# Kernel optimization log

Hardware: AMD Instinct MI355X
Metric: run time of the kernel (lower is better)

Reference implementation:

```python
import jax, jax.numpy as jnp
import numpy as np

LAMBDA_DISCO = 1.0
THRESHOLD = 0.5
EPS = 1e-8
N = 8192


def setup_inputs() -> dict:
    key = jax.random.key(0)
    k1, k2, k3 = jax.random.split(key, 3)
    inputs = jax.random.normal(k1, (N, 1), dtype=jnp.float32)
    targets = jax.random.uniform(k2, (N, 1), dtype=jnp.float32)
    spectators = jax.random.uniform(k3, (N,), dtype=jnp.float32)
    return {"inputs": inputs, "targets": targets, "spectators": spectators}


def _masked_distance_correlation(x, y, m, c):
    """Distance correlation restricted to samples where mask m==1.

    Mathematically identical to filtering x[m], y[m] and running the dense
    dCor (cdist -> double-center -> mean of products), but with fixed shapes
    so it is jit-compatible. c = number of selected samples (>=1).
    """
    # 1-D pairwise L2 distances == |x_i - x_j|   [n, n]
    dx = jnp.abs(x[:, None] - x[None, :])
    dy = jnp.abs(y[:, None] - y[None, :])

    def double_center(D):
        row = (D @ m) / c          # masked row means  [n]
        col = (m @ D) / c          # masked col means  [n]
        tot = (m @ row) / c        # masked total mean (scalar)
        return D - row[:, None] - col[None, :] + tot

    cx = double_center(dx)
    cy = double_center(dy)
    M = m[:, None] * m[None, :]    # pairwise selection mask

    def masked_mean_prod(a, b):
        return jnp.sum(M * a * b) / (c * c)

    dcov_xy = jnp.sqrt(jnp.maximum(masked_mean_prod(cx, cy), EPS))
    dvar_x = jnp.sqrt(jnp.maximum(masked_mean_prod(cx, cx), EPS))
    dvar_y = jnp.sqrt(jnp.maximum(masked_mean_prod(cy, cy), EPS))
    return dcov_xy / (dvar_x * dvar_y)


def reference(inputs, targets, spectators):
    # BCEWithLogitsLoss (mean reduction), numerically stable form.
    x, t = inputs, targets
    bce = jnp.mean(jnp.maximum(x, 0.0) - x * t + jnp.log1p(jnp.exp(-jnp.abs(x))))

    probs = jax.nn.sigmoid(x).reshape(-1)                 # [n]
    m = (spectators >= THRESHOLD).astype(probs.dtype)     # [n] 0/1 mask
    count = jnp.sum(m)
    c_safe = jnp.maximum(count, 1.0)

    dcor = _masked_distance_correlation(probs, spectators, m, c_safe)
    # If no sample passes the condition, return plain BCE.
    return bce + LAMBDA_DISCO * jnp.where(count > 0, dcor, 0.0)
```

## Files before the change

kernel.cpp:

```cpp
#include <hip/hip_runtime.h>
#include <math.h>

#define NTOT 8192
#define THRESH 0.5f
#define EPS_F 1e-8f

#define NSEG 32
#define SEGSZ 256
#define NJG 8
#define SEG_PER_JG (NSEG / NJG)

#define OFF_CNT 0
#define OFF_BCEP 32
#define OFF_TXY 64
#define OFF_TXX 65
#define OFF_TYY 66
#define OFF_SUMS 67
#define OFF_DONE 72
#define OFF_PSS 128
#define OFF_RXP (OFF_PSS + 2 * NTOT)
#define OFF_RYP (OFF_RXP + NJG * NTOT)

__device__ inline float wave_reduce(float v) {
#pragma unroll
    for (int o = 32; o > 0; o >>= 1) v += __shfl_down(v, o, 64);
    return v;
}

__global__ void __launch_bounds__(256) k_stage1(const float* __restrict__ x,
                                                const float* __restrict__ t,
                                                const float* __restrict__ s,
                                                float* __restrict__ ws) {
    __shared__ unsigned wcnt[4];
    __shared__ float wbce[4];
    const int tid = threadIdx.x, b = blockIdx.x;
    const int lane = tid & 63, w = tid >> 6;
    if (b == 0 && tid < 16) ws[OFF_TXY + tid] = 0.f;

    const int i = b * SEGSZ + tid;
    float xi = x[i], ti = t[i], si = s[i];
    float bce = fmaxf(xi, 0.f) - xi * ti + log1pf(expf(-fabsf(xi)));
    bool sel = (si >= THRESH);
    unsigned long long ball = __ballot(sel);
    unsigned pre = __popcll(ball & ((1ull << lane) - 1ull));
    if (lane == 0) wcnt[w] = __popcll(ball);
    float bsum = wave_reduce(bce);
    if (lane == 0) wbce[w] = bsum;
    __syncthreads();
    unsigned off = 0;
#pragma unroll
    for (int k = 0; k < 4; ++k)
        if (k < w) off += wcnt[k];
    if (sel) {
        float p = 1.f / (1.f + expf(-xi));
        ((float2*)(ws + OFF_PSS))[b * SEGSZ + off + pre] = make_float2(p, si);
    }
    if (tid == 0) {
        ((unsigned*)(ws + OFF_CNT))[b] = wcnt[0] + wcnt[1] + wcnt[2] + wcnt[3];
        ws[OFF_BCEP + b] = wbce[0] + wbce[1] + wbce[2] + wbce[3];
    }
}

__global__ void __launch_bounds__(256) k_pairs(float* __restrict__ ws) {
    __shared__ float2 pjs[SEGSZ];
    __shared__ float accs[3];
    const int tid = threadIdx.x;
    const int ib = blockIdx.x & (NSEG - 1);
    const int jg = blockIdx.x >> 5;
    const unsigned* cnt = (const unsigned*)(ws + OFF_CNT);
    const float2* pss = (const float2*)(ws + OFF_PSS);
    const int ci = (int)cnt[ib];
    const bool valid = tid < ci;
    float2 me = valid ? pss[ib * SEGSZ + tid] : make_float2(0.f, 0.f);
    if (tid < 3) accs[tid] = 0.f;

    float rsx = 0.f, rsy = 0.f, t_xy = 0.f, t_xx = 0.f, t_yy = 0.f;
    for (int k = 0; k < SEG_PER_JG; ++k) {
        const int seg = jg * SEG_PER_JG + k;
        const int cj = (int)cnt[seg];
        __syncthreads();
        if (tid < cj) pjs[tid] = pss[seg * SEGSZ + tid];
        __syncthreads();
        if (valid) {
#pragma unroll 8
            for (int j = 0; j < cj; ++j) {
                float2 v = pjs[j];
                float d1 = me.x - v.x;
                float d2 = me.y - v.y;
                float a1 = fabsf(d1);
                float a2 = fabsf(d2);
                rsx += a1;
                rsy += a2;
                t_xy = fmaf(a1, a2, t_xy);
                t_xx = fmaf(d1, d1, t_xx);
                t_yy = fmaf(d2, d2, t_yy);
            }
        }
    }
    const int i = ib * SEGSZ + tid;
    ws[OFF_RXP + jg * NTOT + i] = rsx;
    ws[OFF_RYP + jg * NTOT + i] = rsy;

    t_xy = wave_reduce(t_xy);
    t_xx = wave_reduce(t_xx);
    t_yy = wave_reduce(t_yy);
    if ((tid & 63) == 0) {
        atomicAdd(&accs[0], t_xy);
        atomicAdd(&accs[1], t_xx);
        atomicAdd(&accs[2], t_yy);
    }
    __syncthreads();
    if (tid == 0) {
        atomicAdd(ws + OFF_TXY, accs[0]);
        atomicAdd(ws + OFF_TXX, accs[1]);
        atomicAdd(ws + OFF_TYY, accs[2]);
    }
}

__global__ void __launch_bounds__(256) k_final(float* __restrict__ ws,
                                               float* __restrict__ out) {
    __shared__ float accs[5];
    __shared__ unsigned lastf;
    const int tid = threadIdx.x, b = blockIdx.x;
    const unsigned* cnt = (const unsigned*)(ws + OFF_CNT);
    const int ci = (int)cnt[b];
    const int i = b * SEGSZ + tid;
    float sx = 0, sy = 0, sxy = 0, sxx = 0, syy = 0;
    if (tid < ci) {
        float rx = 0.f, ry = 0.f;
#pragma unroll
        for (int jg = 0; jg < NJG; ++jg) {
            rx += ws[OFF_RXP + jg * NTOT + i];
            ry += ws[OFF_RYP + jg * NTOT + i];
        }
        sx = rx;
        sy = ry;
        sxy = rx * ry;
        sxx = rx * rx;
        syy = ry * ry;
    }
    sx = wave_reduce(sx);
    sy = wave_reduce(sy);
    sxy = wave_reduce(sxy);
    sxx = wave_reduce(sxx);
    syy = wave_reduce(syy);
    if (tid < 5) accs[tid] = 0.f;
    __syncthreads();
    if ((tid & 63) == 0) {
        atomicAdd(&accs[0], sx);
        atomicAdd(&accs[1], sy);
        atomicAdd(&accs[2], sxy);
        atomicAdd(&accs[3], sxx);
        atomicAdd(&accs[4], syy);
    }
    __syncthreads();
    if (tid == 0) {
        atomicAdd(ws + OFF_SUMS + 0, accs[0]);
        atomicAdd(ws + OFF_SUMS + 1, accs[1]);
        atomicAdd(ws + OFF_SUMS + 2, accs[2]);
        atomicAdd(ws + OFF_SUMS + 3, accs[3]);
        atomicAdd(ws + OFF_SUMS + 4, accs[4]);
    }
    __threadfence();
    if (tid == 0) {
        unsigned prev = atomicAdd((unsigned*)(ws + OFF_DONE), 1u);
        lastf = (prev == NSEG - 1) ? 1u : 0u;
    }
    __syncthreads();
    if (!lastf) return;
    __threadfence();
    if (tid == 0) {
        unsigned c = 0;
        float bsum = 0.f;
        for (int k = 0; k < NSEG; ++k) {
            c += cnt[k];
            bsum += ws[OFF_BCEP + k];
        }
        float bce = bsum / (float)NTOT;
        if (c == 0) { out[0] = bce; return; }
        float cf = (float)c;
        float ic2 = 1.f / (cf * cf);
        float ic3 = ic2 / cf;
        float ic4 = ic2 * ic2;
        float Sx = ws[OFF_SUMS + 0], Sy = ws[OFF_SUMS + 1];
        float Vxy = ws[OFF_TXY] * ic2 - 2.f * ws[OFF_SUMS + 2] * ic3 + Sx * Sy * ic4;
        float Vxx = ws[OFF_TXX] * ic2 - 2.f * ws[OFF_SUMS + 3] * ic3 + Sx * Sx * ic4;
        float Vyy = ws[OFF_TYY] * ic2 - 2.f * ws[OFF_SUMS + 4] * ic3 + Sy * Sy * ic4;
        float dcor = sqrtf(fmaxf(Vxy, EPS_F)) /
                     (sqrtf(fmaxf(Vxx, EPS_F)) * sqrtf(fmaxf(Vyy, EPS_F)));
        out[0] = bce + dcor;
    }
}

extern "C" void kernel_launch(void* const* d_in, const int* in_sizes, int n_in,
                              void* d_out, int out_size, void* d_ws, size_t ws_size,
                              hipStream_t stream) {
    const float* x = (const float*)d_in[0];
    const float* t = (const float*)d_in[1];
    const float* s = (const float*)d_in[2];
    float* ws = (float*)d_ws;
    float* out = (float*)d_out;

    k_stage1<<<NSEG, SEGSZ, 0, stream>>>(x, t, s, ws);
    k_pairs<<<NSEG * NJG, SEGSZ, 0, stream>>>(ws);
    k_final<<<NSEG, SEGSZ, 0, stream>>>(ws, out);
}
```

Baseline: 86.47 us.

## Fuse selection stage into pair kernel and replace atomics with single-block final reduction

The compaction and BCE stage is merged into the pairwise kernel. Each block recomputes the sigmoid and mask compaction for its own row segment and for the column segments it visits, so the separate first kernel and its workspace round-trip go away. The global float atomics and last-block counter are replaced by per-block partial slots, which one single-block final kernel reduces. This removes one launch and the global atomics, at the cost of redundant sigmoid and ballot work across blocks and a serial final reduction over the row sums.

```diff
diff --git a/kernel.cpp b/kernel.cpp
--- a/kernel.cpp
+++ b/kernel.cpp
@@ -9,16 +9,12 @@
 #define SEGSZ 256
 #define NJG 8
 #define SEG_PER_JG (NSEG / NJG)
+#define NBLK (NSEG * NJG)
 
 #define OFF_CNT 0
 #define OFF_BCEP 32
-#define OFF_TXY 64
-#define OFF_TXX 65
-#define OFF_TYY 66
-#define OFF_SUMS 67
-#define OFF_DONE 72
-#define OFF_PSS 128
-#define OFF_RXP (OFF_PSS + 2 * NTOT)
+#define OFF_TP 64
+#define OFF_RXP (OFF_TP + 3 * NBLK)
 #define OFF_RYP (OFF_RXP + NJG * NTOT)
 
 __device__ inline float wave_reduce(float v) {
@@ -27,59 +23,64 @@
     return v;
 }
 
-__global__ void __launch_bounds__(256) k_stage1(const float* __restrict__ x,
-                                                const float* __restrict__ t,
-                                                const float* __restrict__ s,
-                                                float* __restrict__ ws) {
+__global__ void __launch_bounds__(256) k_main(const float* __restrict__ x,
+                                              const float* __restrict__ t,
+                                              const float* __restrict__ s,
+                                              float* __restrict__ ws) {
+    __shared__ float2 pjs[SEGSZ];
+    __shared__ float2 mis[SEGSZ];
     __shared__ unsigned wcnt[4];
-    __shared__ float wbce[4];
-    const int tid = threadIdx.x, b = blockIdx.x;
+    __shared__ float wred[4];
+    __shared__ float accs[3];
+    const int tid = threadIdx.x;
     const int lane = tid & 63, w = tid >> 6;
-    if (b == 0 && tid < 16) ws[OFF_TXY + tid] = 0.f;
+    const int ib = blockIdx.x & (NSEG - 1);
+    const int jg = blockIdx.x >> 5;
 
-    const int i = b * SEGSZ + tid;
-    float xi = x[i], ti = t[i], si = s[i];
-    float bce = fmaxf(xi, 0.f) - xi * ti + log1pf(expf(-fabsf(xi)));
-    bool sel = (si >= THRESH);
+    const int gi = ib * SEGSZ + tid;
+    const float xi = x[gi], si = s[gi];
+    const bool sel = (si >= THRESH);
     unsigned long long ball = __ballot(sel);
     unsigned pre = __popcll(ball & ((1ull << lane) - 1ull));
-    if (lane == 0) wcnt[w] = __popcll(ball);
-    float bsum = wave_reduce(bce);
-    if (lane == 0) wbce[w] = bsum;
+    if (lane == 0) wcnt[w] = (unsigned)__popcll(ball);
+    if (tid < 3) accs[tid] = 0.f;
+    if (jg == 0) {
+        float ti = t[gi];
+        float bce = fmaxf(xi, 0.f) - xi * ti + log1pf(expf(-fabsf(xi)));
+        bce = wave_reduce(bce);
+        if (lane == 0) wred[w] = bce;
+    }
     __syncthreads();
     unsigned off = 0;
 #pragma unroll
     for (int k = 0; k < 4; ++k)
         if (k < w) off += wcnt[k];
-    if (sel) {
-        float p = 1.f / (1.f + expf(-xi));
-        ((float2*)(ws + OFF_PSS))[b * SEGSZ + off + pre] = make_float2(p, si);
+    const int ci = (int)(wcnt[0] + wcnt[1] + wcnt[2] + wcnt[3]);
+    if (sel) mis[off + pre] = make_float2(1.f / (1.f + expf(-xi)), si);
+    if (jg == 0 && tid == 0) {
+        ((unsigned*)(ws + OFF_CNT))[ib] = (unsigned)ci;
+        ws[OFF_BCEP + ib] = wred[0] + wred[1] + wred[2] + wred[3];
     }
-    if (tid == 0) {
-        ((unsigned*)(ws + OFF_CNT))[b] = wcnt[0] + wcnt[1] + wcnt[2] + wcnt[3];
-        ws[OFF_BCEP + b] = wbce[0] + wbce[1] + wbce[2] + wbce[3];
-    }
-}
+    __syncthreads();
+    const bool valid = tid < ci;
+    float2 me = mis[tid];
 
-__global__ void __launch_bounds__(256) k_pairs(float* __restrict__ ws) {
-    __shared__ float2 pjs[SEGSZ];
-    __shared__ float accs[3];
-    const int tid = threadIdx.x;
-    const int ib = blockIdx.x & (NSEG - 1);
-    const int jg = blockIdx.x >> 5;
-    const unsigned* cnt = (const unsigned*)(ws + OFF_CNT);
-    const float2* pss = (const float2*)(ws + OFF_PSS);
-    const int ci = (int)cnt[ib];
-    const bool valid = tid < ci;
-    float2 me = valid ? pss[ib * SEGSZ + tid] : make_float2(0.f, 0.f);
-    if (tid < 3) accs[tid] = 0.f;
-
-    float rsx = 0.f, rsy = 0.f, t_xy = 0.f, t_xx = 0.f, t_yy = 0.f;
+    float rsx = 0.f, rsy = 0.f, txy = 0.f, txx = 0.f, tyy = 0.f;
     for (int k = 0; k < SEG_PER_JG; ++k) {
         const int seg = jg * SEG_PER_JG + k;
-        const int cj = (int)cnt[seg];
+        const int gj = seg * SEGSZ + tid;
+        const float xj = x[gj], sj = s[gj];
+        const bool selj = (sj >= THRESH);
+        unsigned long long bj = __ballot(selj);
+        unsigned prej = __popcll(bj & ((1ull << lane) - 1ull));
+        if (lane == 0) wcnt[w] = (unsigned)__popcll(bj);
         __syncthreads();
-        if (tid < cj) pjs[tid] = pss[seg * SEGSZ + tid];
+        unsigned offj = 0;
+#pragma unroll
+        for (int q = 0; q < 4; ++q)
+            if (q < w) offj += wcnt[q];
+        const int cj = (int)(wcnt[0] + wcnt[1] + wcnt[2] + wcnt[3]);
+        if (selj) pjs[offj + prej] = make_float2(1.f / (1.f + expf(-xj)), sj);
         __syncthreads();
         if (valid) {
 #pragma unroll 8
@@ -91,101 +92,85 @@
                 float a2 = fabsf(d2);
                 rsx += a1;
                 rsy += a2;
-                t_xy = fmaf(a1, a2, t_xy);
-                t_xx = fmaf(d1, d1, t_xx);
-                t_yy = fmaf(d2, d2, t_yy);
+                txy = fmaf(a1, a2, txy);
+                txx = fmaf(d1, d1, txx);
+                tyy = fmaf(d2, d2, tyy);
             }
         }
     }
-    const int i = ib * SEGSZ + tid;
-    ws[OFF_RXP + jg * NTOT + i] = rsx;
-    ws[OFF_RYP + jg * NTOT + i] = rsy;
 
-    t_xy = wave_reduce(t_xy);
-    t_xx = wave_reduce(t_xx);
-    t_yy = wave_reduce(t_yy);
-    if ((tid & 63) == 0) {
-        atomicAdd(&accs[0], t_xy);
-        atomicAdd(&accs[1], t_xx);
-        atomicAdd(&accs[2], t_yy);
+    ws[OFF_RXP + jg * NTOT + gi] = rsx;
+    ws[OFF_RYP + jg * NTOT + gi] = rsy;
+
+    txy = wave_reduce(txy);
+    txx = wave_reduce(txx);
+    tyy = wave_reduce(tyy);
+    if (lane == 0) {
+        atomicAdd(&accs[0], txy);
+        atomicAdd(&accs[1], txx);
+        atomicAdd(&accs[2], tyy);
     }
     __syncthreads();
     if (tid == 0) {
-        atomicAdd(ws + OFF_TXY, accs[0]);
-        atomicAdd(ws + OFF_TXX, accs[1]);
-        atomicAdd(ws + OFF_TYY, accs[2]);
+        float* tp = ws + OFF_TP + blockIdx.x * 3;
+        tp[0] = accs[0];
+        tp[1] = accs[1];
+        tp[2] = accs[2];
     }
 }
 
-__global__ void __launch_bounds__(256) k_final(float* __restrict__ ws,
+__global__ void __launch_bounds__(256) k_final(const float* __restrict__ ws,
                                                float* __restrict__ out) {
-    __shared__ float accs[5];
-    __shared__ unsigned lastf;
-    const int tid = threadIdx.x, b = blockIdx.x;
-    const unsigned* cnt = (const unsigned*)(ws + OFF_CNT);
-    const int ci = (int)cnt[b];
-    const int i = b * SEGSZ + tid;
+    __shared__ float red[4][12];
+    const int tid = threadIdx.x;
+    const int lane = tid & 63, w = tid >> 6;
+
     float sx = 0, sy = 0, sxy = 0, sxx = 0, syy = 0;
-    if (tid < ci) {
+    for (int i = tid; i < NTOT; i += 256) {
         float rx = 0.f, ry = 0.f;
 #pragma unroll
         for (int jg = 0; jg < NJG; ++jg) {
             rx += ws[OFF_RXP + jg * NTOT + i];
             ry += ws[OFF_RYP + jg * NTOT + i];
         }
-        sx = rx;
-        sy = ry;
-        sxy = rx * ry;
-        sxx = rx * rx;
-        syy = ry * ry;
+        sx += rx;
+        sy += ry;
+        sxy = fmaf(rx, ry, sxy);
+        sxx = fmaf(rx, rx, sxx);
+        syy = fmaf(ry, ry, syy);
     }
-    sx = wave_reduce(sx);
-    sy = wave_reduce(sy);
-    sxy = wave_reduce(sxy);
-    sxx = wave_reduce(sxx);
-    syy = wave_reduce(syy);
-    if (tid < 5) accs[tid] = 0.f;
-    __syncthreads();
-    if ((tid & 63) == 0) {
-        atomicAdd(&accs[0], sx);
-        atomicAdd(&accs[1], sy);
-        atomicAdd(&accs[2], sxy);
-        atomicAdd(&accs[3], sxx);
-        atomicAdd(&accs[4], syy);
+    const float* tp = ws + OFF_TP + tid * 3;
+    float txy = tp[0], txx = tp[1], tyy = tp[2];
+    float bcep = 0.f, cp = 0.f;
+    if (tid < NSEG) {
+        bcep = ws[OFF_BCEP + tid];
+        cp = (float)((const unsigned*)(ws + OFF_CNT))[tid];
+    }
+
+    float v0 = wave_reduce(sx), v1 = wave_reduce(sy), v2 = wave_reduce(sxy);
+    float v3 = wave_reduce(sxx), v4 = wave_reduce(syy);
+    float v5 = wave_reduce(txy), v6 = wave_reduce(txx), v7 = wave_reduce(tyy);
+    float v8 = wave_reduce(bcep), v9 = wave_reduce(cp);
+    if (lane == 0) {
+        red[w][0] = v0; red[w][1] = v1; red[w][2] = v2; red[w][3] = v3;
+        red[w][4] = v4; red[w][5] = v5; red[w][6] = v6; red[w][7] = v7;
+        red[w][8] = v8; red[w][9] = v9;
     }
     __syncthreads();
     if (tid == 0) {
-        atomicAdd(ws + OFF_SUMS + 0, accs[0]);
-        atomicAdd(ws + OFF_SUMS + 1, accs[1]);
-        atomicAdd(ws + OFF_SUMS + 2, accs[2]);
-        atomicAdd(ws + OFF_SUMS + 3, accs[3]);
-        atomicAdd(ws + OFF_SUMS + 4, accs[4]);
-    }
-    __threadfence();
-    if (tid == 0) {
-        unsigned prev = atomicAdd((unsigned*)(ws + OFF_DONE), 1u);
-        lastf = (prev == NSEG - 1) ? 1u : 0u;
-    }
-    __syncthreads();
-    if (!lastf) return;
-    __threadfence();
-    if (tid == 0) {
-        unsigned c = 0;
-        float bsum = 0.f;
-        for (int k = 0; k < NSEG; ++k) {
-            c += cnt[k];
-            bsum += ws[OFF_BCEP + k];
-        }
-        float bce = bsum / (float)NTOT;
-        if (c == 0) { out[0] = bce; return; }
-        float cf = (float)c;
-        float ic2 = 1.f / (cf * cf);
-        float ic3 = ic2 / cf;
+        float q[10];
+#pragma unroll
+        for (int k = 0; k < 10; ++k)
+            q[k] = red[0][k] + red[1][k] + red[2][k] + red[3][k];
+        float bce = q[8] / (float)NTOT;
+        float c = q[9];
+        if (c == 0.f) { out[0] = bce; return; }
+        float ic2 = 1.f / (c * c);
+        float ic3 = ic2 / c;
         float ic4 = ic2 * ic2;
-        float Sx = ws[OFF_SUMS + 0], Sy = ws[OFF_SUMS + 1];
-        float Vxy = ws[OFF_TXY] * ic2 - 2.f * ws[OFF_SUMS + 2] * ic3 + Sx * Sy * ic4;
-        float Vxx = ws[OFF_TXX] * ic2 - 2.f * ws[OFF_SUMS + 3] * ic3 + Sx * Sx * ic4;
-        float Vyy = ws[OFF_TYY] * ic2 - 2.f * ws[OFF_SUMS + 4] * ic3 + Sy * Sy * ic4;
+        float Vxy = q[5] * ic2 - 2.f * q[2] * ic3 + q[0] * q[1] * ic4;
+        float Vxx = q[6] * ic2 - 2.f * q[3] * ic3 + q[0] * q[0] * ic4;
+        float Vyy = q[7] * ic2 - 2.f * q[4] * ic3 + q[1] * q[1] * ic4;
         float dcor = sqrtf(fmaxf(Vxy, EPS_F)) /
                      (sqrtf(fmaxf(Vxx, EPS_F)) * sqrtf(fmaxf(Vyy, EPS_F)));
         out[0] = bce + dcor;
@@ -201,7 +186,6 @@
     float* ws = (float*)d_ws;
     float* out = (float*)d_out;
 
-    k_stage1<<<NSEG, SEGSZ, 0, stream>>>(x, t, s, ws);
-    k_pairs<<<NSEG * NJG, SEGSZ, 0, stream>>>(ws);
-    k_final<<<NSEG, SEGSZ, 0, stream>>>(ws, out);
+    k_main<<<NBLK, SEGSZ, 0, stream>>>(x, t, s, ws);
+    k_final<<<1, SEGSZ, 0, stream>>>(ws, out);
 }
```

Result: faster. 84.02 us (-2.8%).
